# Optimization experiments

Measured on AMD Instinct MI355X. Metric: run time of the kernel, lower is better.

The kernel has to match this reference:

```python
import jax, jax.numpy as jnp
import numpy as np
import math

V = 1_000_000  # number of mesh vertices
J = 23         # number of joints (fixed by kintree_table in source)
PARENTS = np.array([-1, 0, 1, 1, 3, 4, 5, 4, 7, 4, 9, 1, 11, 12, 13, 12, 15, 12, 17, 0, 19, 0, 21])


def setup_inputs() -> dict:
    key = jax.random.key(0)
    ks = jax.random.split(key, 16)
    v_template = jax.random.normal(ks[0], (1, V, 3), jnp.float32) * 0.5
    w = jax.random.uniform(ks[1], (1, V, J), jnp.float32)
    skinning = w / w.sum(-1, keepdims=True)  # rows sum to 1 like LBS weights
    joints_rest = jax.random.normal(ks[2], (1, J, 3), jnp.float32) * 0.3
    jp = lambda i: jax.random.normal(ks[3 + i], (1, 3), jnp.float32) * 0.1
    return {
        'v_template': v_template,
        'skinning': skinning,
        'joints_rest': joints_rest,
        'joint_0': jp(0), 'joint_1': jp(1), 'joint_2': jp(2), 'joint_3': jp(3),
        'joint_4': jp(4), 'joint_5': jp(5), 'joint_12': jp(6), 'joint_13': jp(7),
        'local_adjust': jax.random.normal(ks[11], (1, V, 3), jnp.float32) * 0.01,
        'displacement': jax.random.normal(ks[12], (1, 1, 3), jnp.float32) * 0.01,
        'scale': jnp.ones((1,), jnp.float32),
        'estimated_location': jax.random.normal(ks[13], (1, 3), jnp.float32),
        'batch_size': 4,
    }


def rodrigues(r):
    # r: [J,3] axis-angle -> [J,3,3] rotation matrices
    angle = jnp.sqrt(jnp.sum(r * r, axis=-1, keepdims=True) + 1e-12)  # [J,1]
    axis = r / angle
    x, y, z = axis[:, 0], axis[:, 1], axis[:, 2]
    zero = jnp.zeros_like(x)
    K = jnp.stack([zero, -z, y, z, zero, -x, -y, x, zero], axis=-1).reshape(-1, 3, 3)
    s = jnp.sin(angle)[..., None]
    c = jnp.cos(angle)[..., None]
    I = jnp.eye(3, dtype=r.dtype)
    return I + s * K + (1.0 - c) * (K @ K)


def build_pose_tensor(joint_0, joint_1, joint_2, joint_3, joint_4, joint_5, joint_12, joint_13):
    pi = math.pi
    pose = jnp.zeros((J, 3), jnp.float32)
    pose = pose.at[0].set(pi / 2 * jnp.tanh(joint_0[0]))
    pose = pose.at[1].set(pi / 4 * jnp.tanh(joint_1[0]))
    pose = pose.at[2].set(pi / 9 * jnp.tanh(joint_2[0]))
    pose = pose.at[3].set(pi / 3 * jnp.tanh(joint_3[0]))
    pose = pose.at[11].set(pi / 3 * jnp.tanh(joint_3[0]) * jnp.array([1.0, -1.0, -1.0], jnp.float32))
    pose = pose.at[4].set(pi / 3 * jnp.tanh(joint_4[0]))
    pose = pose.at[12].set(pi / 3 * jnp.tanh(joint_12[0]))
    pose = pose.at[13].set(pi / 3 * jnp.tanh(joint_13[0]))
    pose = pose.at[5].set(pi / 3 * jnp.tanh(joint_5[0]))
    return pose


def lbs(verts, joints, pose):
    # verts: [V,3], joints: [J,3], pose: [J,3] axis-angle
    R = rodrigues(pose)  # [J,3,3]
    rel = joints.at[1:].add(-joints[PARENTS[1:]])  # parent-relative joint offsets
    # local 4x4 transforms
    T_local = jnp.zeros((J, 4, 4), verts.dtype)
    T_local = T_local.at[:, :3, :3].set(R)
    T_local = T_local.at[:, :3, 3].set(rel)
    T_local = T_local.at[:, 3, 3].set(1.0)
    # compose along kinematic tree (fixed 23-joint chain -> small static loop)
    G = [T_local[0]]
    for j in range(1, J):
        G.append(G[PARENTS[j]] @ T_local[j])
    G = jnp.stack(G)  # [J,4,4]
    posed_joints = G[:, :3, 3]
    # remove rest-pose joint locations: A = G * [[I,-j],[0,1]]
    t_corr = jnp.einsum('jab,jb->ja', G[:, :3, :3], joints)
    A = G.at[:, :3, 3].add(-t_corr)  # [J,4,4]
    # skin vertices: per-vertex blended transform
    T = (skinning_ref[0] @ A.reshape(J, 16)).reshape(-1, 4, 4) if False else None
    return A, posed_joints


def reference(v_template, skinning, joints_rest, joint_0, joint_1, joint_2, joint_3,
              joint_4, joint_5, joint_12, joint_13, local_adjust, displacement,
              scale, estimated_location, batch_size):
    pose = build_pose_tensor(joint_0, joint_1, joint_2, joint_3, joint_4, joint_5,
                             joint_12, joint_13)
    verts = v_template[0] + 0.1 * jnp.tanh(local_adjust[0])  # [V,3]
    joints = joints_rest[0]  # [J,3]
    A, posed_joints = lbs(verts, joints, pose)
    # weighted per-vertex transforms: [V,J] @ [J,16] -> [V,4,4]  (memory-bound)
    Tv = (skinning[0] @ A.reshape(J, 16)).reshape(-1, 4, 4)
    v_h = jnp.concatenate([verts, jnp.ones((verts.shape[0], 1), verts.dtype)], axis=-1)
    verts_posed = jnp.einsum('vab,vb->va', Tv, v_h)[:, :3]  # [V,3]
    disp = 0.1 * jnp.tanh(displacement[0, 0])  # [3]
    loc = estimated_location[0]  # [3]
    verts_out = 0.0035 * scale[0] * verts_posed + loc + disp  # [V,3]
    joints_out = 0.0035 * scale[0] * posed_joints + loc + disp  # [J,3]
    verts_batched = jnp.broadcast_to(verts_out[None], (batch_size,) + verts_out.shape)
    return verts_batched, pose, joints_out, scale, displacement, local_adjust
```

## Files before the change

kernel.cpp:

```cpp
#include <hip/hip_runtime.h>

#define V_N 1000000
#define J_N 23
#define BLK 256
#define NFULL 3906

#define OUT_POSE   12000000
#define OUT_JOINTS 12000069
#define OUT_SCALE  12000138
#define OUT_DISP   12000139
#define OUT_LA     12000142

__device__ __constant__ int c_parents[J_N] = {
    -1, 0, 1, 1, 3, 4, 5, 4, 7, 4, 9, 1, 11, 12, 13, 12, 15, 12, 17, 0, 19, 0, 21
};

__global__ void stage1_kernel(
    const float* __restrict__ joints_rest,
    const float* __restrict__ j0, const float* __restrict__ j1,
    const float* __restrict__ j2, const float* __restrict__ j3,
    const float* __restrict__ j4, const float* __restrict__ j5,
    const float* __restrict__ j12, const float* __restrict__ j13,
    const float* __restrict__ disp, const float* __restrict__ scale,
    const float* __restrict__ loc,
    float* __restrict__ wsA, float* __restrict__ out)
{
    __shared__ float jr[J_N][3];
    __shared__ float pose[J_N][3];
    __shared__ float R[J_N][9];
    __shared__ float rel[J_N][3];
    __shared__ float G[J_N][12];
    __shared__ float sb[4];
    const int t = threadIdx.x;

    if (t < J_N * 3) {
        ((float*)jr)[t]   = joints_rest[t];
        ((float*)pose)[t] = 0.0f;
    }
    __syncthreads();

    if (t < 27) {
        const float PI = 3.14159265358979323846f;
        const int   rows[9] = { 0, 1, 2, 3, 11, 4, 5, 12, 13 };
        const float cf[9]   = { PI/2, PI/4, PI/9, PI/3, PI/3, PI/3, PI/3, PI/3, PI/3 };
        int i = t / 3, cmp = t % 3;
        const float* srcs[9];
        srcs[0]=j0; srcs[1]=j1; srcs[2]=j2; srcs[3]=j3; srcs[4]=j3;
        srcs[5]=j4; srcs[6]=j5; srcs[7]=j12; srcs[8]=j13;
        float syz = (rows[i] == 11 && cmp > 0) ? -1.0f : 1.0f;
        pose[rows[i]][cmp] = cf[i] * syz * tanhf(srcs[i][cmp]);
    }
    if (t == 32) {
        sb[0] = 0.0035f * scale[0];
        sb[1] = loc[0] + 0.1f * tanhf(disp[0]);
        sb[2] = loc[1] + 0.1f * tanhf(disp[1]);
        sb[3] = loc[2] + 0.1f * tanhf(disp[2]);
    }
    __syncthreads();

    if (t < J_N) {
        float rx = pose[t][0], ry = pose[t][1], rz = pose[t][2];
        float ang = sqrtf(rx*rx + ry*ry + rz*rz + 1e-12f);
        float inv = 1.0f / ang;
        float x = rx * inv, y = ry * inv, z = rz * inv;
        float s = sinf(ang), c = cosf(ang);
        float K[9]  = { 0.f, -z, y,  z, 0.f, -x,  -y, x, 0.f };
        float K2[9];
        for (int r = 0; r < 3; r++)
            for (int cc = 0; cc < 3; cc++) {
                float a = 0.f;
                for (int k = 0; k < 3; k++) a += K[r*3+k] * K[k*3+cc];
                K2[r*3+cc] = a;
            }
        for (int r = 0; r < 3; r++)
            for (int cc = 0; cc < 3; cc++) {
                float id = (r == cc) ? 1.f : 0.f;
                R[t][r*3+cc] = id + s * K[r*3+cc] + (1.f - c) * K2[r*3+cc];
            }
        int p = c_parents[t];
        for (int cc = 0; cc < 3; cc++)
            rel[t][cc] = (p < 0) ? jr[t][cc] : (jr[t][cc] - jr[p][cc]);
    }
    __syncthreads();

    if (t == 0) {
        for (int r = 0; r < 3; r++) {
            for (int cc = 0; cc < 3; cc++) G[0][r*4+cc] = R[0][r*3+cc];
            G[0][r*4+3] = rel[0][r];
        }
        for (int j = 1; j < J_N; j++) {
            int p = c_parents[j];
            for (int r = 0; r < 3; r++) {
                float g0 = G[p][r*4+0], g1 = G[p][r*4+1], g2 = G[p][r*4+2], g3 = G[p][r*4+3];
                for (int cc = 0; cc < 3; cc++)
                    G[j][r*4+cc] = g0*R[j][0*3+cc] + g1*R[j][1*3+cc] + g2*R[j][2*3+cc];
                G[j][r*4+3] = g0*rel[j][0] + g1*rel[j][1] + g2*rel[j][2] + g3;
            }
        }
    }
    __syncthreads();

    if (t < J_N) {
        for (int r = 0; r < 3; r++) {
            float tc = G[t][r*4+0]*jr[t][0] + G[t][r*4+1]*jr[t][1] + G[t][r*4+2]*jr[t][2];
            wsA[t*12 + r*4 + 0] = G[t][r*4+0];
            wsA[t*12 + r*4 + 1] = G[t][r*4+1];
            wsA[t*12 + r*4 + 2] = G[t][r*4+2];
            wsA[t*12 + r*4 + 3] = G[t][r*4+3] - tc;
            out[OUT_JOINTS + t*3 + r] = sb[0] * G[t][r*4+3] + sb[1+r];
        }
    }
    if (t < J_N * 3) out[OUT_POSE + t] = ((const float*)pose)[t];
    if (t == 0) {
        wsA[276] = sb[0]; wsA[277] = sb[1]; wsA[278] = sb[2]; wsA[279] = sb[3];
        out[OUT_SCALE]  = scale[0];
        out[OUT_DISP+0] = disp[0]; out[OUT_DISP+1] = disp[1]; out[OUT_DISP+2] = disp[2];
    }
}

__global__ void stage2_kernel(
    const float* __restrict__ vt,
    const float* __restrict__ skin,
    const float* __restrict__ la,
    const float* __restrict__ wsA,
    const int* __restrict__ bsp,
    float* __restrict__ out)
{
    __shared__ uint4 s_sk[1472];

    const int tid = threadIdx.x;
    const int blk = blockIdx.x;
    const int v0  = blk * BLK;
    const int v   = v0 + tid;

    const uint4* g = (const uint4*)skin + (size_t)blk * 1472;

    float tvx = 0.f, tvy = 0.f, tvz = 0.f;
    float lx  = 0.f, ly  = 0.f, lz  = 0.f;

    if (blk < NFULL) {
        uint4 r0 = g[tid];
        uint4 r1 = g[tid + 256];
        uint4 r2 = g[tid + 512];
        uint4 r3 = g[tid + 768];
        uint4 r4 = g[tid + 1024];
        uint4 r5;
        if (tid < 192) r5 = g[tid + 1280];
        const float* vp = vt + (size_t)v * 3;
        const float* lp = la + (size_t)v * 3;
        tvx = vp[0]; tvy = vp[1]; tvz = vp[2];
        lx  = lp[0]; ly  = lp[1]; lz  = lp[2];

        s_sk[tid]        = r0;
        s_sk[tid + 256]  = r1;
        s_sk[tid + 512]  = r2;
        s_sk[tid + 768]  = r3;
        s_sk[tid + 1024] = r4;
        if (tid < 192) s_sk[tid + 1280] = r5;
    } else {
        for (int i = tid; i < 368; i += BLK) s_sk[i] = g[i];
        if (v < V_N) {
            const float* vp = vt + (size_t)v * 3;
            const float* lp = la + (size_t)v * 3;
            tvx = vp[0]; tvy = vp[1]; tvz = vp[2];
            lx  = lp[0]; ly  = lp[1]; lz  = lp[2];
        }
    }
    __syncthreads();

    if (v < V_N) {
        const float* wr = (const float*)s_sk + tid * J_N;
        float acc[12];
        #pragma unroll
        for (int k = 0; k < 12; k++) acc[k] = 0.f;
        #pragma unroll
        for (int j = 0; j < J_N; j++) {
            float w = wr[j];
            const float* Aj = wsA + j * 12;
            #pragma unroll
            for (int k = 0; k < 12; k++) acc[k] = fmaf(w, Aj[k], acc[k]);
        }
        float vx = tvx + 0.1f * tanhf(lx);
        float vy = tvy + 0.1f * tanhf(ly);
        float vz = tvz + 0.1f * tanhf(lz);
        float px = acc[0]*vx + acc[1]*vy + acc[2]*vz  + acc[3];
        float py = acc[4]*vx + acc[5]*vy + acc[6]*vz  + acc[7];
        float pz = acc[8]*vx + acc[9]*vy + acc[10]*vz + acc[11];
        float s  = wsA[276];
        float ox = fmaf(s, px, wsA[277]);
        float oy = fmaf(s, py, wsA[278]);
        float oz = fmaf(s, pz, wsA[279]);

        const int bsz = bsp[0];
        float* ob = out + (size_t)v * 3;
        for (int b = 0; b < bsz; b++) {
            ob[0] = ox; ob[1] = oy; ob[2] = oz;
            ob += 3000000;
        }
        float* oe = out + OUT_LA + (size_t)v * 3;
        oe[0] = lx; oe[1] = ly; oe[2] = lz;
    }
}

extern "C" void kernel_launch(void* const* d_in, const int* in_sizes, int n_in,
                              void* d_out, int out_size, void* d_ws, size_t ws_size,
                              hipStream_t stream) {
    const float* vt   = (const float*)d_in[0];
    const float* skin = (const float*)d_in[1];
    const float* jr   = (const float*)d_in[2];
    const float* j0   = (const float*)d_in[3];
    const float* j1   = (const float*)d_in[4];
    const float* j2   = (const float*)d_in[5];
    const float* j3   = (const float*)d_in[6];
    const float* j4   = (const float*)d_in[7];
    const float* j5   = (const float*)d_in[8];
    const float* j12  = (const float*)d_in[9];
    const float* j13  = (const float*)d_in[10];
    const float* la   = (const float*)d_in[11];
    const float* disp = (const float*)d_in[12];
    const float* sc   = (const float*)d_in[13];
    const float* loc  = (const float*)d_in[14];
    const int* bs     = (const int*)d_in[15];

    float* wsA = (float*)d_ws;
    float* out = (float*)d_out;

    stage1_kernel<<<1, 128, 0, stream>>>(jr, j0, j1, j2, j3, j4, j5, j12, j13,
                                         disp, sc, loc, wsA, out);
    stage2_kernel<<<(V_N + BLK - 1) / BLK, BLK, 0, stream>>>(vt, skin, la, wsA, bs, out);
}
```

Measured before the change: 220.6 us.

## Make skinning kernel persistent with per-wave register prefetch of next tile

```diff
diff --git a/kernel.cpp b/kernel.cpp
--- a/kernel.cpp
+++ b/kernel.cpp
@@ -3,7 +3,8 @@
 #define V_N 1000000
 #define J_N 23
 #define BLK 256
-#define NFULL 3906
+#define NT_TILES 3907
+#define GRID2 1536
 
 #define OUT_POSE   12000000
 #define OUT_JOINTS 12000069
@@ -126,79 +127,109 @@
     const int* __restrict__ bsp,
     float* __restrict__ out)
 {
-    __shared__ uint4 s_sk[1472];
-
-    const int tid = threadIdx.x;
-    const int blk = blockIdx.x;
-    const int v0  = blk * BLK;
-    const int v   = v0 + tid;
-
-    const uint4* g = (const uint4*)skin + (size_t)blk * 1472;
-
-    float tvx = 0.f, tvy = 0.f, tvz = 0.f;
-    float lx  = 0.f, ly  = 0.f, lz  = 0.f;
-
-    if (blk < NFULL) {
-        uint4 r0 = g[tid];
-        uint4 r1 = g[tid + 256];
-        uint4 r2 = g[tid + 512];
-        uint4 r3 = g[tid + 768];
-        uint4 r4 = g[tid + 1024];
-        uint4 r5;
-        if (tid < 192) r5 = g[tid + 1280];
-        const float* vp = vt + (size_t)v * 3;
-        const float* lp = la + (size_t)v * 3;
-        tvx = vp[0]; tvy = vp[1]; tvz = vp[2];
-        lx  = lp[0]; ly  = lp[1]; lz  = lp[2];
-
-        s_sk[tid]        = r0;
-        s_sk[tid + 256]  = r1;
-        s_sk[tid + 512]  = r2;
-        s_sk[tid + 768]  = r3;
-        s_sk[tid + 1024] = r4;
-        if (tid < 192) s_sk[tid + 1280] = r5;
-    } else {
-        for (int i = tid; i < 368; i += BLK) s_sk[i] = g[i];
-        if (v < V_N) {
-            const float* vp = vt + (size_t)v * 3;
-            const float* lp = la + (size_t)v * 3;
-            tvx = vp[0]; tvy = vp[1]; tvz = vp[2];
-            lx  = lp[0]; ly  = lp[1]; lz  = lp[2];
-        }
-    }
-    __syncthreads();
-
-    if (v < V_N) {
-        const float* wr = (const float*)s_sk + tid * J_N;
-        float acc[12];
-        #pragma unroll
-        for (int k = 0; k < 12; k++) acc[k] = 0.f;
-        #pragma unroll
-        for (int j = 0; j < J_N; j++) {
-            float w = wr[j];
-            const float* Aj = wsA + j * 12;
+    __shared__ uint4 s_sk[4][368];
+
+    const int tid  = threadIdx.x;
+    const int lane = tid & 63;
+    const int w    = tid >> 6;
+    uint4* const slice = s_sk[w];
+    const float* const wsl = (const float*)s_sk[w];
+
+    const float sc = wsA[276];
+    const float bx = wsA[277], by = wsA[278], bz = wsA[279];
+    const int   bsz = bsp[0];
+
+    int t = blockIdx.x;
+    float cvx = 0.f, cvy = 0.f, cvz = 0.f, clx = 0.f, cly = 0.f, clz = 0.f;
+
+    {
+        const int vb = t * 256 + (w << 6);
+        const uint4* g = (const uint4*)(skin + (size_t)vb * 23);
+        uint4 r0 = g[lane];
+        uint4 r1 = g[lane + 64];
+        uint4 r2 = g[lane + 128];
+        uint4 r3 = g[lane + 192];
+        uint4 r4 = g[lane + 256];
+        uint4 r5 = make_uint4(0u, 0u, 0u, 0u);
+        if (lane < 48) r5 = g[lane + 320];
+        const float* vp = vt + (size_t)(vb + lane) * 3;
+        const float* lp = la + (size_t)(vb + lane) * 3;
+        cvx = vp[0]; cvy = vp[1]; cvz = vp[2];
+        clx = lp[0]; cly = lp[1]; clz = lp[2];
+        slice[lane]       = r0;
+        slice[lane + 64]  = r1;
+        slice[lane + 128] = r2;
+        slice[lane + 192] = r3;
+        slice[lane + 256] = r4;
+        if (lane < 48) slice[lane + 320] = r5;
+    }
+
+    for (;;) {
+        const int tn  = t + GRID2;
+        const int vbn = tn * 256 + (w << 6);
+        const bool actn = (tn < NT_TILES) && (vbn < V_N);
+        uint4 n0 = make_uint4(0u,0u,0u,0u), n1 = n0, n2 = n0, n3 = n0, n4 = n0, n5 = n0;
+        float nvx = 0.f, nvy = 0.f, nvz = 0.f, nlx = 0.f, nly = 0.f, nlz = 0.f;
+        if (actn) {
+            const uint4* g = (const uint4*)(skin + (size_t)vbn * 23);
+            n0 = g[lane];
+            n1 = g[lane + 64];
+            n2 = g[lane + 128];
+            n3 = g[lane + 192];
+            n4 = g[lane + 256];
+            if (lane < 48) n5 = g[lane + 320];
+            const float* vp = vt + (size_t)(vbn + lane) * 3;
+            const float* lp = la + (size_t)(vbn + lane) * 3;
+            nvx = vp[0]; nvy = vp[1]; nvz = vp[2];
+            nlx = lp[0]; nly = lp[1]; nlz = lp[2];
+        }
+
+        const int vb = t * 256 + (w << 6);
+        if (vb < V_N) {
+            const int v = vb + lane;
+            const float* wr = wsl + lane * J_N;
+            float acc[12];
             #pragma unroll
-            for (int k = 0; k < 12; k++) acc[k] = fmaf(w, Aj[k], acc[k]);
-        }
-        float vx = tvx + 0.1f * tanhf(lx);
-        float vy = tvy + 0.1f * tanhf(ly);
-        float vz = tvz + 0.1f * tanhf(lz);
-        float px = acc[0]*vx + acc[1]*vy + acc[2]*vz  + acc[3];
-        float py = acc[4]*vx + acc[5]*vy + acc[6]*vz  + acc[7];
-        float pz = acc[8]*vx + acc[9]*vy + acc[10]*vz + acc[11];
-        float s  = wsA[276];
-        float ox = fmaf(s, px, wsA[277]);
-        float oy = fmaf(s, py, wsA[278]);
-        float oz = fmaf(s, pz, wsA[279]);
-
-        const int bsz = bsp[0];
-        float* ob = out + (size_t)v * 3;
-        for (int b = 0; b < bsz; b++) {
-            ob[0] = ox; ob[1] = oy; ob[2] = oz;
-            ob += 3000000;
-        }
-        float* oe = out + OUT_LA + (size_t)v * 3;
-        oe[0] = lx; oe[1] = ly; oe[2] = lz;
+            for (int k = 0; k < 12; k++) acc[k] = 0.f;
+            #pragma unroll
+            for (int j = 0; j < J_N; j++) {
+                const float wj = wr[j];
+                const float* Aj = wsA + j * 12;
+                #pragma unroll
+                for (int k = 0; k < 12; k++) acc[k] = fmaf(wj, Aj[k], acc[k]);
+            }
+            const float vx = cvx + 0.1f * tanhf(clx);
+            const float vy = cvy + 0.1f * tanhf(cly);
+            const float vz = cvz + 0.1f * tanhf(clz);
+            const float px = acc[0]*vx + acc[1]*vy + acc[2]*vz  + acc[3];
+            const float py = acc[4]*vx + acc[5]*vy + acc[6]*vz  + acc[7];
+            const float pz = acc[8]*vx + acc[9]*vy + acc[10]*vz + acc[11];
+            const float ox = fmaf(sc, px, bx);
+            const float oy = fmaf(sc, py, by);
+            const float oz = fmaf(sc, pz, bz);
+
+            float* ob = out + (size_t)v * 3;
+            for (int b = 0; b < bsz; b++) {
+                ob[0] = ox; ob[1] = oy; ob[2] = oz;
+                ob += 3000000;
+            }
+            float* oe = out + OUT_LA + (size_t)v * 3;
+            oe[0] = clx; oe[1] = cly; oe[2] = clz;
+        }
+
+        if (tn >= NT_TILES) break;
+
+        if (actn) {
+            slice[lane]       = n0;
+            slice[lane + 64]  = n1;
+            slice[lane + 128] = n2;
+            slice[lane + 192] = n3;
+            slice[lane + 256] = n4;
+            if (lane < 48) slice[lane + 320] = n5;
+            cvx = nvx; cvy = nvy; cvz = nvz;
+            clx = nlx; cly = nly; clz = nlz;
+        }
+        t = tn;
     }
 }
 
@@ -227,5 +258,5 @@
 
     stage1_kernel<<<1, 128, 0, stream>>>(jr, j0, j1, j2, j3, j4, j5, j12, j13,
                                          disp, sc, loc, wsA, out);
-    stage2_kernel<<<(V_N + BLK - 1) / BLK, BLK, 0, stream>>>(vt, skin, la, wsA, bs, out);
+    stage2_kernel<<<GRID2, BLK, 0, stream>>>(vt, skin, la, wsA, bs, out);
 }
```

Measured after the change: 221.7 us. About the same (+0.5%).
